# Kernel tuning notes

Measured on AMD Instinct MI355X. Metric: run time of the kernel, lower is better.

Reference implementation:

```python
import jax, jax.numpy as jnp
import numpy as np

EMBED_DIM = 1024
NUM_HEADS = 16
HEAD_DIM = EMBED_DIM // NUM_HEADS
T, B = 2048, 2


def setup_inputs() -> dict:
    key = jax.random.key(0)
    ks = jax.random.split(key, 12)
    s = 1.0 / np.sqrt(EMBED_DIM)
    x = jax.random.normal(ks[0], (T, B, EMBED_DIM), dtype=jnp.float32)
    time_decay = jax.random.uniform(ks[1], (T, B, 1), dtype=jnp.float32)
    # causal mask: masked_fill where mask == 0
    attn_mask = jnp.tril(jnp.ones((T, T), dtype=jnp.int32))
    Wq = jax.random.uniform(ks[2], (EMBED_DIM, EMBED_DIM), jnp.float32, -s, s)
    bq = jax.random.uniform(ks[3], (EMBED_DIM,), jnp.float32, -s, s)
    Wk = jax.random.uniform(ks[4], (EMBED_DIM, EMBED_DIM), jnp.float32, -s, s)
    bk = jax.random.uniform(ks[5], (EMBED_DIM,), jnp.float32, -s, s)
    Wv = jax.random.uniform(ks[6], (EMBED_DIM, EMBED_DIM), jnp.float32, -s, s)
    bv = jax.random.uniform(ks[7], (EMBED_DIM,), jnp.float32, -s, s)
    Wo = jax.random.uniform(ks[8], (EMBED_DIM, EMBED_DIM), jnp.float32, -s, s)
    bo = jax.random.uniform(ks[9], (EMBED_DIM,), jnp.float32, -s, s)
    return {"x": x, "time_decay": time_decay, "attn_mask": attn_mask,
            "Wq": Wq, "bq": bq, "Wk": Wk, "bk": bk,
            "Wv": Wv, "bv": bv, "Wo": Wo, "bo": bo}


def reference(x, time_decay, attn_mask, Wq, bq, Wk, bk, Wv, bv, Wo, bo):
    t, b, e = x.shape
    h, d = NUM_HEADS, HEAD_DIM
    # linear (torch: y = x @ W.T + b), then split heads -> (B, H, T, D)
    def proj(W, bias):
        y = jnp.einsum('tbe,fe->tbf', x, W) + bias
        return y.reshape(t, b, h, d).transpose(1, 2, 0, 3)
    Q, K, V = proj(Wq, bq), proj(Wk, bk), proj(Wv, bv)
    scores = jnp.einsum('bhqd,bhkd->bhqk', Q, K) / np.sqrt(d).astype(jnp.float32)
    scores = jnp.where(attn_mask == 0, jnp.float32(-1e9), scores)
    attn = jax.nn.softmax(scores, axis=-1)
    out = jnp.einsum('bhqk,bhkd->bhqd', attn, V)      # (B,H,T,D)
    out = out.transpose(2, 0, 1, 3).reshape(t, b, e)   # (T,B,E)
    out = jnp.einsum('tbe,fe->tbf', out, Wo) + bo
    return out * time_decay
```

## Files before the change

### kernel.cpp

```cpp
#include <hip/hip_runtime.h>


typedef unsigned short u16;
typedef __attribute__((ext_vector_type(8))) short bf16x8_t;
typedef __attribute__((ext_vector_type(4))) float fx4_t;

#define T_SEQ 2048
#define BATCH 2
#define EMB   1024
#define NH    16
#define HD    64
#define MROWS (T_SEQ * BATCH)

#define EXP2F(x) __builtin_amdgcn_exp2f(x)

__device__ __forceinline__ float bf2f(u16 u) {
  union { unsigned int i; float f; } v;
  v.i = ((unsigned int)u) << 16;
  return v.f;
}
__device__ __forceinline__ u16 f2bf(float f) {
  union { float f; unsigned int i; } v;
  v.f = f;
  unsigned int x = v.i;
  unsigned int r = (x + 0x7fffu + ((x >> 16) & 1u)) >> 16;
  return (u16)r;
}

__device__ __forceinline__ void glds16(const void* g, void* l) {
  __builtin_amdgcn_global_load_lds(
      (const __attribute__((address_space(1))) unsigned int*)g,
      (__attribute__((address_space(3))) unsigned int*)l, 16, 0, 0);
}


__global__ void cvt_all(const float* __restrict__ x,
                        const float* __restrict__ wq, const float* __restrict__ wk,
                        const float* __restrict__ wv, const float* __restrict__ wo,
                        u16* __restrict__ xb,
                        u16* __restrict__ wqb, u16* __restrict__ wkb,
                        u16* __restrict__ wvb, u16* __restrict__ wob) {
  int i = blockIdx.x * blockDim.x + threadIdx.x;
  const float* src; u16* dst; int off;
  if (i < 1048576)      { src = x;  dst = xb;  off = i; }
  else if (i < 1310720) { src = wq; dst = wqb; off = i - 1048576; }
  else if (i < 1572864) { src = wk; dst = wkb; off = i - 1310720; }
  else if (i < 1835008) { src = wv; dst = wvb; off = i - 1572864; }
  else                  { src = wo; dst = wob; off = i - 1835008; }
  float4 v = ((const float4*)src)[off];
  ushort4 o;
  o.x = f2bf(v.x); o.y = f2bf(v.y); o.z = f2bf(v.z); o.w = f2bf(v.w);
  ((ushort4*)dst)[off] = o;
}

__global__ __launch_bounds__(256, 2) void gemm_qkv(
    const u16* __restrict__ xb,
    const u16* __restrict__ wq, const u16* __restrict__ wk, const u16* __restrict__ wv,
    const float* __restrict__ bq, const float* __restrict__ bk, const float* __restrict__ bv,
    u16* __restrict__ Qm, u16* __restrict__ Km, u16* __restrict__ VTg) {
  __shared__ short As[128 * 64];
  __shared__ short Bs[128 * 64];

  const int z = blockIdx.z;
  const u16* W = (z == 0) ? wq : (z == 1) ? wk : wv;
  const float* bias = (z == 0) ? bq : (z == 1) ? bk : bv;

  const int tid = threadIdx.x;
  const int bm = blockIdx.x, bn = blockIdx.y;
  const int lane = tid & 63, w = tid >> 6;
  const int wm = w >> 1, wn = w & 1;
  const int lr = lane & 15, quad = lane >> 4;
  const int r0 = lane >> 3;
  const int c8s = ((lane & 7) ^ r0) * 8;
  const int sw = (lr & 7);

  fx4_t acc[4][4];
#pragma unroll
  for (int i = 0; i < 4; i++)
#pragma unroll
    for (int j = 0; j < 4; j++) acc[i][j] = (fx4_t){0.f, 0.f, 0.f, 0.f};

  for (int k0 = 0; k0 < EMB; k0 += 64) {
#pragma unroll
    for (int i = 0; i < 4; i++) {
      const int rr = w * 32 + i * 8;
      const int ml = bm * 128 + rr + r0;
      const int grow = (z == 2) ? (((ml & 2047) << 1) | (ml >> 11)) : ml;
      glds16(xb + (size_t)grow * EMB + k0 + c8s, &As[rr * 64]);
      glds16(W + (size_t)(bn * 128 + rr + r0) * EMB + k0 + c8s, &Bs[rr * 64]);
    }
    __syncthreads();
#pragma unroll
    for (int ks = 0; ks < 2; ++ks) {
      bf16x8_t a[4], b[4];
#pragma unroll
      for (int i = 0; i < 4; i++)
        a[i] = *(const bf16x8_t*)&As[(wm * 64 + i * 16 + lr) * 64 + (((ks * 4 + quad) ^ sw) * 8)];
#pragma unroll
      for (int j = 0; j < 4; j++)
        b[j] = *(const bf16x8_t*)&Bs[(wn * 64 + j * 16 + lr) * 64 + (((ks * 4 + quad) ^ sw) * 8)];
      if (z == 2) {
#pragma unroll
        for (int i = 0; i < 4; i++)
#pragma unroll
          for (int j = 0; j < 4; j++)
            acc[i][j] = __builtin_amdgcn_mfma_f32_16x16x32_bf16(b[j], a[i], acc[i][j], 0, 0, 0);
      } else {
#pragma unroll
        for (int i = 0; i < 4; i++)
#pragma unroll
          for (int j = 0; j < 4; j++)
            acc[i][j] = __builtin_amdgcn_mfma_f32_16x16x32_bf16(a[i], b[j], acc[i][j], 0, 0, 0);
      }
    }
    __syncthreads();
  }

  if (z == 2) {
#pragma unroll
    for (int i = 0; i < 4; i++) {
#pragma unroll
      for (int j = 0; j < 4; j++) {
#pragma unroll
        for (int r = 0; r < 4; r++) {
          const int n = bn * 128 + wn * 64 + j * 16 + quad * 4 + r;
          const int ml = bm * 128 + wm * 64 + i * 16 + lr;
          const int t = ml & 2047, bb = ml >> 11;
          const int h = n >> 6, d = n & 63;
          VTg[((size_t)(bb * NH + h) * HD + d) * T_SEQ + t] = f2bf(acc[i][j][r] + bias[n]);
        }
      }
    }
  } else {
    u16* dst = (z == 0) ? Qm : Km;
#pragma unroll
    for (int i = 0; i < 4; i++) {
#pragma unroll
      for (int j = 0; j < 4; j++) {
        const int n = bn * 128 + wn * 64 + j * 16 + lr;
        const float bsv = bias[n];
#pragma unroll
        for (int r = 0; r < 4; r++) {
          const int m = bm * 128 + wm * 64 + i * 16 + quad * 4 + r;
          dst[(size_t)m * EMB + n] = f2bf(acc[i][j][r] + bsv);
        }
      }
    }
  }
}

__global__ __launch_bounds__(256, 2) void gemm_out(
    const u16* __restrict__ Ob, const u16* __restrict__ wo,
    const float* __restrict__ bo, const float* __restrict__ td,
    float* __restrict__ out) {
  __shared__ short As[64 * 64];
  __shared__ short Bs[128 * 64];

  const int tid = threadIdx.x;
  const int bm = blockIdx.x, bn = blockIdx.y;
  const int lane = tid & 63, w = tid >> 6;
  const int wm = w >> 1, wn = w & 1;
  const int lr = lane & 15, quad = lane >> 4;
  const int r0 = lane >> 3;
  const int c8s = ((lane & 7) ^ r0) * 8;
  const int sw = (lr & 7);

  fx4_t acc[2][4];
#pragma unroll
  for (int i = 0; i < 2; i++)
#pragma unroll
    for (int j = 0; j < 4; j++) acc[i][j] = (fx4_t){0.f, 0.f, 0.f, 0.f};

  for (int k0 = 0; k0 < EMB; k0 += 64) {
#pragma unroll
    for (int i = 0; i < 2; i++) {
      const int rr = w * 16 + i * 8;
      glds16(Ob + (size_t)(bm * 64 + rr + r0) * EMB + k0 + c8s, &As[rr * 64]);
    }
#pragma unroll
    for (int i = 0; i < 4; i++) {
      const int rr = w * 32 + i * 8;
      glds16(wo + (size_t)(bn * 128 + rr + r0) * EMB + k0 + c8s, &Bs[rr * 64]);
    }
    __syncthreads();
#pragma unroll
    for (int ks = 0; ks < 2; ++ks) {
      bf16x8_t a[2], b[4];
#pragma unroll
      for (int i = 0; i < 2; i++)
        a[i] = *(const bf16x8_t*)&As[(wm * 32 + i * 16 + lr) * 64 + (((ks * 4 + quad) ^ sw) * 8)];
#pragma unroll
      for (int j = 0; j < 4; j++)
        b[j] = *(const bf16x8_t*)&Bs[(wn * 64 + j * 16 + lr) * 64 + (((ks * 4 + quad) ^ sw) * 8)];
#pragma unroll
      for (int i = 0; i < 2; i++)
#pragma unroll
        for (int j = 0; j < 4; j++)
          acc[i][j] = __builtin_amdgcn_mfma_f32_16x16x32_bf16(a[i], b[j], acc[i][j], 0, 0, 0);
    }
    __syncthreads();
  }

#pragma unroll
  for (int i = 0; i < 2; i++) {
#pragma unroll
    for (int j = 0; j < 4; j++) {
      const int n = bn * 128 + wn * 64 + j * 16 + lr;
      const float bsv = bo[n];
#pragma unroll
      for (int r = 0; r < 4; r++) {
        const int m = bm * 64 + wm * 32 + i * 16 + quad * 4 + r;
        out[(size_t)m * EMB + n] = (acc[i][j][r] + bsv) * td[m];
      }
    }
  }
}

__global__ __launch_bounds__(256, 3) void attn_mfma6(
    const u16* __restrict__ Qm, const u16* __restrict__ Km, const u16* __restrict__ VTg,
    u16* __restrict__ Ob) {
  __shared__ short Kd[2][64 * 64];
  __shared__ short Vd[2][64 * 64];
  __shared__ short Ps[4][16 * 72];

  const int blk = blockIdx.x;
  const int bh = blk & 31;
  const int j = blk >> 5;
  const int qt = (j & 1) ? (31 - (j >> 1)) : (j >> 1);
  const int qb = qt * 64;
  const int b = bh >> 4, h = bh & 15;

  const int tid = threadIdx.x;
  const int w = tid >> 6, lane = tid & 63;
  const int lr = lane & 15, quad = lane >> 4;
  const int r0 = lane >> 3;
  const int c8s = ((lane & 7) ^ r0) * 8;
  const int sw = (lr & 7);

  const u16* Qbase = Qm + (size_t)b * EMB + (size_t)h * HD;
  const u16* Kbase = Km + (size_t)b * EMB + (size_t)h * HD;
  const u16* VTb = VTg + (size_t)bh * HD * T_SEQ;

  const float QSCALE = 0.18033688f;
  bf16x8_t qf[2];
#pragma unroll
  for (int ks = 0; ks < 2; ks++) {
    bf16x8_t v = *(const bf16x8_t*)(Qbase + (size_t)(qb + w * 16 + lr) * 2 * EMB + ks * 32 + quad * 8);
    bf16x8_t o;
#pragma unroll
    for (int e = 0; e < 8; e++) o[e] = (short)f2bf(bf2f((u16)v[e]) * QSCALE);
    qf[ks] = o;
  }

  fx4_t acc_o[4];
#pragma unroll
  for (int dn = 0; dn < 4; dn++) acc_o[dn] = (fx4_t){0.f, 0.f, 0.f, 0.f};
  float m_i = -1e30f, l_i = 0.f;

#define STAGE(kt_, buf_)                                                            \
  {                                                                                 \
    const int k0_ = (kt_) * 64;                                                     \
    _Pragma("unroll")                                                               \
    for (int i = 0; i < 2; i++) {                                                   \
      const int rr = w * 16 + i * 8;                                                \
      glds16(Kbase + (size_t)(k0_ + rr + r0) * 2 * EMB + c8s, &Kd[buf_][rr * 64]);  \
      glds16(VTb + (size_t)(rr + r0) * T_SEQ + k0_ + c8s, &Vd[buf_][rr * 64]);      \
    }                                                                               \
  }

  const int nkt = qt + 1;
  STAGE(0, 0);
  __syncthreads();

  for (int kt = 0; kt < nkt; kt++) {
    const int buf = kt & 1;
    if (kt + 1 < nkt) STAGE(kt + 1, buf ^ 1);

    fx4_t st[4];
#pragma unroll
    for (int nt = 0; nt < 4; nt++) st[nt] = (fx4_t){0.f, 0.f, 0.f, 0.f};
#pragma unroll
    for (int ks = 0; ks < 2; ks++) {
#pragma unroll
      for (int nt = 0; nt < 4; nt++) {
        bf16x8_t kf = *(const bf16x8_t*)&Kd[buf][(nt * 16 + lr) * 64 + (((ks * 4 + quad) ^ sw) * 8)];
        st[nt] = __builtin_amdgcn_mfma_f32_16x16x32_bf16(kf, qf[ks], st[nt], 0, 0, 0);
      }
    }

    if (kt == qt) {
#pragma unroll
      for (int nt = 0; nt < 4; nt++)
#pragma unroll
        for (int r = 0; r < 4; r++)
          if (nt * 16 + quad * 4 + r > w * 16 + lr) st[nt][r] = -1e30f;
    }

    float rmax = -1e30f;
#pragma unroll
    for (int nt = 0; nt < 4; nt++)
#pragma unroll
      for (int r = 0; r < 4; r++) rmax = fmaxf(rmax, st[nt][r]);
    rmax = fmaxf(rmax, __shfl_xor(rmax, 16));
    rmax = fmaxf(rmax, __shfl_xor(rmax, 32));
    const float mn = fmaxf(m_i, rmax);
    const float alpha = EXP2F(m_i - mn);
    m_i = mn;
    float rsum = 0.f;
#pragma unroll
    for (int nt = 0; nt < 4; nt++) {
#pragma unroll
      for (int r = 0; r < 4; r++) {
        float e = EXP2F(st[nt][r] - mn);
        st[nt][r] = e;
        rsum += e;
      }
    }
    rsum += __shfl_xor(rsum, 16);
    rsum += __shfl_xor(rsum, 32);
    l_i = l_i * alpha + rsum;

    short* Pw = Ps[w];
#pragma unroll
    for (int nt = 0; nt < 4; nt++) {
      short4 pv;
      pv.x = (short)f2bf(st[nt][0]);
      pv.y = (short)f2bf(st[nt][1]);
      pv.z = (short)f2bf(st[nt][2]);
      pv.w = (short)f2bf(st[nt][3]);
      *(short4*)&Pw[lr * 72 + nt * 16 + quad * 4] = pv;
    }

#pragma unroll
    for (int r = 0; r < 4; r++) {
      const float a_r = __shfl(alpha, quad * 4 + r);
#pragma unroll
      for (int dn = 0; dn < 4; dn++) acc_o[dn][r] *= a_r;
    }

#pragma unroll
    for (int ks = 0; ks < 2; ks++) {
      bf16x8_t pf = *(const bf16x8_t*)&Pw[lr * 72 + ks * 32 + quad * 8];
#pragma unroll
      for (int dn = 0; dn < 4; dn++) {
        bf16x8_t vf = *(const bf16x8_t*)&Vd[buf][(dn * 16 + lr) * 64 + (((ks * 4 + quad) ^ sw) * 8)];
        acc_o[dn] = __builtin_amdgcn_mfma_f32_16x16x32_bf16(pf, vf, acc_o[dn], 0, 0, 0);
      }
    }

    __syncthreads();
  }
#undef STAGE

  const float inv = 1.0f / l_i;
#pragma unroll
  for (int r = 0; r < 4; r++) {
    const float inv_r = __shfl(inv, quad * 4 + r);
    const int t = qb + w * 16 + quad * 4 + r;
#pragma unroll
    for (int dn = 0; dn < 4; dn++) {
      const int d = dn * 16 + lr;
      Ob[(size_t)(t * BATCH + b) * EMB + h * HD + d] = f2bf(acc_o[dn][r] * inv_r);
    }
  }
}

extern "C" void kernel_launch(void* const* d_in, const int* in_sizes, int n_in,
                              void* d_out, int out_size, void* d_ws, size_t ws_size,
                              hipStream_t stream) {
  const float* x  = (const float*)d_in[0];
  const float* td = (const float*)d_in[1];
  const float* Wq = (const float*)d_in[3];
  const float* bq = (const float*)d_in[4];
  const float* Wk = (const float*)d_in[5];
  const float* bk = (const float*)d_in[6];
  const float* Wv = (const float*)d_in[7];
  const float* bv = (const float*)d_in[8];
  const float* Wo = (const float*)d_in[9];
  const float* bo = (const float*)d_in[10];
  float* out = (float*)d_out;

  char* ws = (char*)d_ws;
  u16* xb  = (u16*)(ws + 0);
  u16* wqb = (u16*)(ws + ((size_t)8  << 20));
  u16* wkb = (u16*)(ws + ((size_t)10 << 20));
  u16* wvb = (u16*)(ws + ((size_t)12 << 20));
  u16* wob = (u16*)(ws + ((size_t)14 << 20));
  u16* Qm  = (u16*)(ws + ((size_t)16 << 20));
  u16* Km  = (u16*)(ws + ((size_t)24 << 20));
  u16* VTg = (u16*)(ws + ((size_t)32 << 20));
  u16* Ob  = xb;

  cvt_all<<<8192, 256, 0, stream>>>(x, Wq, Wk, Wv, Wo, xb, wqb, wkb, wvb, wob);

  gemm_qkv<<<dim3(MROWS / 128, EMB / 128, 3), 256, 0, stream>>>(
      xb, wqb, wkb, wvb, bq, bk, bv, Qm, Km, VTg);

  attn_mfma6<<<1024, 256, 0, stream>>>(Qm, Km, VTg, Ob);

  gemm_out<<<dim3(MROWS / 64, EMB / 128), 256, 0, stream>>>(Ob, wob, bo, td, out);
}
```

Measured before the change: 204.6 us.

## Load K/V fragments directly from global memory, drop LDS staging and block syncs

The attention kernel no longer stages K and V tiles into double-buffered shared memory. Each wave now loads its MFMA operand fragments straight from global memory (relying on cache), which removes the per-iteration __syncthreads and frees LDS so occupancy can rise to 4 blocks per CU. P is packed to bf16 by truncation instead of round-to-nearest. The risk is that four waves each re-read the same K/V rows from L2 instead of sharing one LDS copy, and truncation slightly lowers precision.

```diff
diff --git a/kernel.cpp b/kernel.cpp
--- a/kernel.cpp
+++ b/kernel.cpp
@@ -2,6 +2,7 @@
 
 
 typedef unsigned short u16;
+typedef unsigned int u32;
 typedef __attribute__((ext_vector_type(8))) short bf16x8_t;
 typedef __attribute__((ext_vector_type(4))) float fx4_t;
 
@@ -25,6 +26,9 @@
   unsigned int x = v.i;
   unsigned int r = (x + 0x7fffu + ((x >> 16) & 1u)) >> 16;
   return (u16)r;
+}
+__device__ __forceinline__ u32 fbits(float f) {
+  union { float f; u32 i; } v; v.f = f; return v.i;
 }
 
 __device__ __forceinline__ void glds16(const void* g, void* l) {
@@ -216,11 +220,9 @@
   }
 }
 
-__global__ __launch_bounds__(256, 3) void attn_mfma6(
+__global__ __launch_bounds__(256, 4) void attn_mfma7(
     const u16* __restrict__ Qm, const u16* __restrict__ Km, const u16* __restrict__ VTg,
     u16* __restrict__ Ob) {
-  __shared__ short Kd[2][64 * 64];
-  __shared__ short Vd[2][64 * 64];
   __shared__ short Ps[4][16 * 72];
 
   const int blk = blockIdx.x;
@@ -233,9 +235,6 @@
   const int tid = threadIdx.x;
   const int w = tid >> 6, lane = tid & 63;
   const int lr = lane & 15, quad = lane >> 4;
-  const int r0 = lane >> 3;
-  const int c8s = ((lane & 7) ^ r0) * 8;
-  const int sw = (lr & 7);
 
   const u16* Qbase = Qm + (size_t)b * EMB + (size_t)h * HD;
   const u16* Kbase = Km + (size_t)b * EMB + (size_t)h * HD;
@@ -257,24 +256,11 @@
   for (int dn = 0; dn < 4; dn++) acc_o[dn] = (fx4_t){0.f, 0.f, 0.f, 0.f};
   float m_i = -1e30f, l_i = 0.f;
 
-#define STAGE(kt_, buf_)                                                            \
-  {                                                                                 \
-    const int k0_ = (kt_) * 64;                                                     \
-    _Pragma("unroll")                                                               \
-    for (int i = 0; i < 2; i++) {                                                   \
-      const int rr = w * 16 + i * 8;                                                \
-      glds16(Kbase + (size_t)(k0_ + rr + r0) * 2 * EMB + c8s, &Kd[buf_][rr * 64]);  \
-      glds16(VTb + (size_t)(rr + r0) * T_SEQ + k0_ + c8s, &Vd[buf_][rr * 64]);      \
-    }                                                                               \
-  }
-
+  short* Pw = Ps[w];
   const int nkt = qt + 1;
-  STAGE(0, 0);
-  __syncthreads();
 
   for (int kt = 0; kt < nkt; kt++) {
-    const int buf = kt & 1;
-    if (kt + 1 < nkt) STAGE(kt + 1, buf ^ 1);
+    const int k0 = kt * 64;
 
     fx4_t st[4];
 #pragma unroll
@@ -283,10 +269,17 @@
     for (int ks = 0; ks < 2; ks++) {
 #pragma unroll
       for (int nt = 0; nt < 4; nt++) {
-        bf16x8_t kf = *(const bf16x8_t*)&Kd[buf][(nt * 16 + lr) * 64 + (((ks * 4 + quad) ^ sw) * 8)];
+        bf16x8_t kf = *(const bf16x8_t*)(Kbase + (size_t)(k0 + nt * 16 + lr) * 2 * EMB + ks * 32 + quad * 8);
         st[nt] = __builtin_amdgcn_mfma_f32_16x16x32_bf16(kf, qf[ks], st[nt], 0, 0, 0);
       }
     }
+
+    bf16x8_t vf[2][4];
+#pragma unroll
+    for (int ks = 0; ks < 2; ks++)
+#pragma unroll
+      for (int dn = 0; dn < 4; dn++)
+        vf[ks][dn] = *(const bf16x8_t*)(VTb + (size_t)(dn * 16 + lr) * T_SEQ + k0 + ks * 32 + quad * 8);
 
     if (kt == qt) {
 #pragma unroll
@@ -320,15 +313,12 @@
     rsum += __shfl_xor(rsum, 32);
     l_i = l_i * alpha + rsum;
 
-    short* Pw = Ps[w];
 #pragma unroll
     for (int nt = 0; nt < 4; nt++) {
-      short4 pv;
-      pv.x = (short)f2bf(st[nt][0]);
-      pv.y = (short)f2bf(st[nt][1]);
-      pv.z = (short)f2bf(st[nt][2]);
-      pv.w = (short)f2bf(st[nt][3]);
-      *(short4*)&Pw[lr * 72 + nt * 16 + quad * 4] = pv;
+      u32 p01 = (fbits(st[nt][0]) >> 16) | (fbits(st[nt][1]) & 0xFFFF0000u);
+      u32 p23 = (fbits(st[nt][2]) >> 16) | (fbits(st[nt][3]) & 0xFFFF0000u);
+      uint2 pv; pv.x = p01; pv.y = p23;
+      *(uint2*)&Pw[lr * 72 + nt * 16 + quad * 4] = pv;
     }
 
 #pragma unroll
@@ -342,15 +332,10 @@
     for (int ks = 0; ks < 2; ks++) {
       bf16x8_t pf = *(const bf16x8_t*)&Pw[lr * 72 + ks * 32 + quad * 8];
 #pragma unroll
-      for (int dn = 0; dn < 4; dn++) {
-        bf16x8_t vf = *(const bf16x8_t*)&Vd[buf][(dn * 16 + lr) * 64 + (((ks * 4 + quad) ^ sw) * 8)];
-        acc_o[dn] = __builtin_amdgcn_mfma_f32_16x16x32_bf16(pf, vf, acc_o[dn], 0, 0, 0);
-      }
-    }
-
-    __syncthreads();
-  }
-#undef STAGE
+      for (int dn = 0; dn < 4; dn++)
+        acc_o[dn] = __builtin_amdgcn_mfma_f32_16x16x32_bf16(pf, vf[ks][dn], acc_o[dn], 0, 0, 0);
+    }
+  }
 
   const float inv = 1.0f / l_i;
 #pragma unroll
@@ -396,7 +381,7 @@
   gemm_qkv<<<dim3(MROWS / 128, EMB / 128, 3), 256, 0, stream>>>(
       xb, wqb, wkb, wvb, bq, bk, bv, Qm, Km, VTg);
 
-  attn_mfma6<<<1024, 256, 0, stream>>>(Qm, Km, VTg, Ob);
+  attn_mfma7<<<1024, 256, 0, stream>>>(Qm, Km, VTg, Ob);
 
   gemm_out<<<dim3(MROWS / 64, EMB / 128), 256, 0, stream>>>(Ob, wob, bo, td, out);
 }
```

New measurement: 341.0 us. 1.67x slower.
